# Kernel tuning notes

Measured on AMD Instinct MI355X. Metric: run time of the kernel, lower is better.

Reference implementation:

```python
import jax, jax.numpy as jnp
import numpy as np

BEV_H, BEV_W, BEV_Z = 128, 128, 16
N_VOX = BEV_H * BEV_W * BEV_Z  # 262144
C = 128
N_UNMASKED = N_VOX // 4       # 65536 seed voxels (proposal > 0)
LN_EPS = 1e-5
NEG_SLOPE = 0.01


def setup_inputs() -> dict:
    key = jax.random.key(0)
    ks = jax.random.split(key, 8)
    x3d = jax.random.normal(ks[0], (1, C, N_VOX), dtype=jnp.float32)
    # disjoint unmasked/masked index sets from a permutation (proposal mask)
    perm = jax.random.permutation(ks[1], N_VOX)
    unmasked_idx = jnp.sort(perm[:N_UNMASKED]).astype(jnp.int32)
    masked_idx = jnp.sort(perm[N_UNMASKED:]).astype(jnp.int32)
    s = 0.05
    return {
        "x3d": x3d,
        "w1": jax.random.normal(ks[2], (C, C // 2), jnp.float32) * s,
        "b1": jnp.zeros((C // 2,), jnp.float32),
        "ln_g": jnp.ones((C // 2,), jnp.float32),
        "ln_b": jnp.zeros((C // 2,), jnp.float32),
        "w2": jax.random.normal(ks[3], (C // 2, C), jnp.float32) * s,
        "b2": jnp.zeros((C,), jnp.float32),
        "sdb_w": jax.random.normal(ks[4], (C, C // 2), jnp.float32) * s,
        "sdb_b": jnp.zeros((C // 2,), jnp.float32),
        "ssc_w": jax.random.normal(ks[5], (C // 2, 20), jnp.float32) * s,
        "ssc_b": jnp.zeros((20,), jnp.float32),
        "aux_w": jax.random.normal(ks[6], (C, 20), jnp.float32) * s,
        "aux_b": jnp.zeros((20,), jnp.float32),
        "unmasked_idx": unmasked_idx,
        "masked_idx": masked_idx,
    }


def _leaky(x):
    return jnp.where(x > 0, x, NEG_SLOPE * x)


def _layernorm(x, g, b):
    mu = jnp.mean(x, axis=-1, keepdims=True)
    var = jnp.mean(jnp.square(x - mu), axis=-1, keepdims=True)
    return (x - mu) * jax.lax.rsqrt(var + LN_EPS) * g + b


def reference(x3d, w1, b1, ln_g, ln_b, w2, b2, sdb_w, sdb_b, ssc_w, ssc_b,
              aux_w, aux_b, unmasked_idx, masked_idx):
    feats = x3d[0].T  # [N_vox, C]
    # gather seed (unmasked) voxel features; SGB treated as identity stand-in
    seed_feats = feats[unmasked_idx]            # [Nu, C]
    # gather masked voxel features and infill with mlp_prior:
    # Linear -> LayerNorm -> LeakyReLU -> Linear
    m = feats[masked_idx]                       # [Nm, C]
    h = _leaky(_layernorm(m @ w1 + b1, ln_g, ln_b))
    prior = h @ w2 + b2                         # [Nm, C]
    # scatter both into the dense voxel grid
    vox = jnp.zeros((N_VOX, C), x3d.dtype)
    vox = vox.at[unmasked_idx].set(seed_feats).at[masked_idx].set(prior)
    # SDB dense decode stand-in: pointwise conv C -> C/2 + LeakyReLU
    d = _leaky(vox @ sdb_w + sdb_b)             # [N_vox, C/2]
    # ssc head: per-voxel logits -> [1, 20, H, W, Z]
    ssc = d @ ssc_w + ssc_b                     # [N_vox, 20]
    ssc_logit = ssc.reshape(BEV_H, BEV_W, BEV_Z, 20).transpose(3, 0, 1, 2)[None]
    # aux sparse head on seed features
    sem_logit = seed_feats @ aux_w + aux_b      # [Nu, 20]
    return ssc_logit, sem_logit
```

## Files before the change

kernel.cpp:

```cpp
#include <hip/hip_runtime.h>
#include <hip/hip_bf16.h>


#define NVOX 262144
#define NU   65536
#define NM   196608
#define CIN  128
#define CHALF 64
#define NCLS 20
#define TR   64
#define NBLK (NVOX / TR)

#define SXS 136
#define SHS 68
#define SOS 21

#define W1F  0
#define W2F  8192
#define SDBF 16384
#define SSCF 24576
#define AUXF 26624
#define WS_WT 30720

typedef unsigned short u16;
typedef short    bf16x4 __attribute__((ext_vector_type(4)));
typedef short    bf16x8 __attribute__((ext_vector_type(8)));
typedef float    f32x4  __attribute__((ext_vector_type(4)));

__device__ __forceinline__ u16 f2b(float f) {
    __hip_bfloat16 h = __float2bfloat16(f);
    return *(u16*)&h;
}

__global__ void prep_weights(const float* __restrict__ w1,  const float* __restrict__ w2,
                             const float* __restrict__ sdbw,const float* __restrict__ sscw,
                             const float* __restrict__ auxw,
                             const int* __restrict__ uidx,  const int* __restrict__ midx,
                             u16* __restrict__ ws) {
    int i = blockIdx.x * blockDim.x + threadIdx.x;
    const int stride = gridDim.x * blockDim.x;
    int* __restrict__ rank = (int*)(ws + WS_WT);
    for (int t = i; t < NU; t += stride) rank[uidx[t]] = t;
    for (int t = i; t < NM; t += stride) rank[midx[t]] = -1;
    for (; i < WS_WT; i += stride) {
        float v;
        if (i < W2F) {
            int t = i, j = t & 7, lane = (t >> 3) & 63, kc = (t >> 9) & 3, nt = t >> 11;
            int k = kc*32 + (lane >> 4)*8 + j, n = nt*16 + (lane & 15);
            v = w1[k*CHALF + n];
        } else if (i < SDBF) {
            int t = i - W2F, j = t & 7, lane = (t >> 3) & 63, kc = (t >> 9) & 1, nt = t >> 10;
            int k = kc*32 + (lane >> 4)*8 + j, n = nt*16 + (lane & 15);
            v = w2[k*CIN + n];
        } else if (i < SSCF) {
            int t = i - SDBF, j = t & 7, lane = (t >> 3) & 63, kc = (t >> 9) & 3, nt = t >> 11;
            int k = kc*32 + (lane >> 4)*8 + j, n = nt*16 + (lane & 15);
            v = sdbw[k*CHALF + n];
        } else if (i < AUXF) {
            int t = i - SSCF, j = t & 7, lane = (t >> 3) & 63, kc = (t >> 9) & 1, nt = t >> 10;
            int k = kc*32 + (lane >> 4)*8 + j, n = nt*16 + (lane & 15);
            v = (n < NCLS) ? sscw[k*NCLS + n] : 0.f;
        } else {
            int t = i - AUXF, j = t & 7, lane = (t >> 3) & 63, kc = (t >> 9) & 3, nt = t >> 11;
            int k = kc*32 + (lane >> 4)*8 + j, n = nt*16 + (lane & 15);
            v = (n < NCLS) ? auxw[k*NCLS + n] : 0.f;
        }
        ws[i] = f2b(v);
    }
}

__global__ __launch_bounds__(512, 8)
void sgn_mfma(const float* __restrict__ x3d,
              const float* __restrict__ b1,   const float* __restrict__ lng,
              const float* __restrict__ lnb,  const float* __restrict__ bb2,
              const float* __restrict__ sdbb, const float* __restrict__ sscb,
              const float* __restrict__ auxb,
              const int* __restrict__ rank,   const u16* __restrict__ wt,
              float* __restrict__ out)
{
    __shared__ __align__(16) u16 sX[TR * SXS];
    __shared__ __align__(16) u16 sH[TR * SHS];
    __shared__ __align__(16) float sOut[TR * SOS];
    __shared__ float sLN[TR][2][2];
    __shared__ int sRank[TR];

    const int tid = threadIdx.x;
    const int p0  = (int)blockIdx.x * TR;

    {
        const int gch = (tid >> 4) * 4;
        const int vp  = (tid & 15) * 4;
        f32x4 cv[4];
        #pragma unroll
        for (int r = 0; r < 4; ++r)
            cv[r] = *(const f32x4*)&x3d[(size_t)(gch + r) * NVOX + p0 + vp];
        #pragma unroll
        for (int j = 0; j < 4; ++j) {
            bf16x4 row;
            #pragma unroll
            for (int r = 0; r < 4; ++r) ((u16*)&row)[r] = f2b(cv[r][j]);
            *(bf16x4*)&sX[(vp + j) * SXS + gch] = row;
        }
    }
    if (tid < TR) sRank[tid] = rank[p0 + tid];
    __syncthreads();

    const int w    = tid >> 6;
    const int half = w & 1;
    const int m0   = (w >> 1) * 16;
    const int lane = tid & 63;
    const int q    = lane >> 4;
    const int n15  = lane & 15;
    const int kq   = q * 8;

    {
        const int ntb = half * 2;
        f32x4 acc[2];
        #pragma unroll
        for (int i = 0; i < 2; ++i) {
            const float b = b1[(ntb + i)*16 + n15];
            acc[i] = (f32x4){b, b, b, b};
        }
        bf16x8 af[4];
        #pragma unroll
        for (int kc = 0; kc < 4; ++kc)
            af[kc] = *(const bf16x8*)&sX[(m0 + n15) * SXS + kc*32 + kq];
        #pragma unroll
        for (int h2 = 0; h2 < 2; ++h2) {
            bf16x8 bf[4];
            #pragma unroll
            for (int kk = 0; kk < 2; ++kk)
                #pragma unroll
                for (int i = 0; i < 2; ++i)
                    bf[kk*2 + i] = *(const bf16x8*)&wt[W1F + (((ntb+i)*4 + (2*h2+kk))*64 + lane)*8];
            #pragma unroll
            for (int kk = 0; kk < 2; ++kk)
                #pragma unroll
                for (int i = 0; i < 2; ++i)
                    acc[i] = __builtin_amdgcn_mfma_f32_16x16x32_bf16(af[2*h2+kk], bf[kk*2+i], acc[i], 0, 0, 0);
        }
        float s1v[4], s2v[4];
        #pragma unroll
        for (int reg = 0; reg < 4; ++reg) {
            float s1 = acc[0][reg] + acc[1][reg];
            float s2 = acc[0][reg]*acc[0][reg] + acc[1][reg]*acc[1][reg];
            #pragma unroll
            for (int m = 1; m <= 8; m <<= 1) {
                s1 += __shfl_xor(s1, m, 64);
                s2 += __shfl_xor(s2, m, 64);
            }
            s1v[reg] = s1; s2v[reg] = s2;
        }
        if (n15 == 0) {
            #pragma unroll
            for (int reg = 0; reg < 4; ++reg) {
                const int row = m0 + q*4 + reg;
                sLN[row][half][0] = s1v[reg];
                sLN[row][half][1] = s2v[reg];
            }
        }
        __syncthreads();
        float gv[2], ev[2];
        #pragma unroll
        for (int i = 0; i < 2; ++i) { gv[i] = lng[(ntb+i)*16 + n15]; ev[i] = lnb[(ntb+i)*16 + n15]; }
        #pragma unroll
        for (int reg = 0; reg < 4; ++reg) {
            const int row = m0 + q*4 + reg;
            const float s1 = s1v[reg] + sLN[row][half^1][0];
            const float s2 = s2v[reg] + sLN[row][half^1][1];
            const float mu  = s1 * (1.f/64.f);
            const float var = s2 * (1.f/64.f) - mu*mu;
            const float rs  = rsqrtf(var + 1e-5f);
            #pragma unroll
            for (int i = 0; i < 2; ++i) {
                float h = (acc[i][reg] - mu) * rs * gv[i] + ev[i];
                h = h > 0.f ? h : 0.01f*h;
                sH[row * SHS + (ntb+i)*16 + n15] = f2b(h);
            }
        }
    }
    __syncthreads();

    {
        const int ntb2 = half * 4;
        f32x4 acc2[4];
        #pragma unroll
        for (int i = 0; i < 4; ++i) {
            const float b = bb2[(ntb2 + i)*16 + n15];
            acc2[i] = (f32x4){b, b, b, b};
        }
        bf16x8 af2[2];
        #pragma unroll
        for (int kc = 0; kc < 2; ++kc)
            af2[kc] = *(const bf16x8*)&sH[(m0 + n15) * SHS + kc*32 + kq];
        #pragma unroll
        for (int kc = 0; kc < 2; ++kc) {
            bf16x8 bf[4];
            #pragma unroll
            for (int i = 0; i < 4; ++i)
                bf[i] = *(const bf16x8*)&wt[W2F + (((ntb2+i)*2 + kc)*64 + lane)*8];
            #pragma unroll
            for (int i = 0; i < 4; ++i)
                acc2[i] = __builtin_amdgcn_mfma_f32_16x16x32_bf16(af2[kc], bf[i], acc2[i], 0, 0, 0);
        }
        #pragma unroll
        for (int reg = 0; reg < 4; ++reg) {
            const int row = m0 + q*4 + reg;
            if (sRank[row] < 0) {
                #pragma unroll
                for (int i = 0; i < 4; ++i)
                    sX[row * SXS + (ntb2+i)*16 + n15] = f2b(acc2[i][reg]);
            }
        }
    }
    __syncthreads();

    {
        const int ntb = half * 2;
        f32x4 accd[2];
        #pragma unroll
        for (int i = 0; i < 2; ++i) {
            const float b = sdbb[(ntb + i)*16 + n15];
            accd[i] = (f32x4){b, b, b, b};
        }
        bf16x8 af[4];
        #pragma unroll
        for (int kc = 0; kc < 4; ++kc)
            af[kc] = *(const bf16x8*)&sX[(m0 + n15) * SXS + kc*32 + kq];
        #pragma unroll
        for (int h2 = 0; h2 < 2; ++h2) {
            bf16x8 bf[4];
            #pragma unroll
            for (int kk = 0; kk < 2; ++kk)
                #pragma unroll
                for (int i = 0; i < 2; ++i)
                    bf[kk*2 + i] = *(const bf16x8*)&wt[SDBF + (((ntb+i)*4 + (2*h2+kk))*64 + lane)*8];
            #pragma unroll
            for (int kk = 0; kk < 2; ++kk)
                #pragma unroll
                for (int i = 0; i < 2; ++i)
                    accd[i] = __builtin_amdgcn_mfma_f32_16x16x32_bf16(af[2*h2+kk], bf[kk*2+i], accd[i], 0, 0, 0);
        }
        #pragma unroll
        for (int reg = 0; reg < 4; ++reg) {
            const int row = m0 + q*4 + reg;
            #pragma unroll
            for (int i = 0; i < 2; ++i) {
                float vv = accd[i][reg];
                vv = vv > 0.f ? vv : 0.01f*vv;
                sH[row * SHS + (ntb+i)*16 + n15] = f2b(vv);
            }
        }
    }
    __syncthreads();

    {
        f32x4 accs;
        {
            const int col = half*16 + n15;
            const float b = (col < NCLS) ? sscb[col] : 0.f;
            accs = (f32x4){b, b, b, b};
        }
        bf16x8 af2[2];
        #pragma unroll
        for (int kc = 0; kc < 2; ++kc)
            af2[kc] = *(const bf16x8*)&sH[(m0 + n15) * SHS + kc*32 + kq];
        bf16x8 bf[2];
        #pragma unroll
        for (int kc = 0; kc < 2; ++kc)
            bf[kc] = *(const bf16x8*)&wt[SSCF + ((half*2 + kc)*64 + lane)*8];
        #pragma unroll
        for (int kc = 0; kc < 2; ++kc)
            accs = __builtin_amdgcn_mfma_f32_16x16x32_bf16(af2[kc], bf[kc], accs, 0, 0, 0);
        #pragma unroll
        for (int reg = 0; reg < 4; ++reg) {
            const int row = m0 + q*4 + reg;
            if (half == 0)      sOut[row*SOS + n15] = accs[reg];
            else if (n15 < 4)   sOut[row*SOS + 16 + n15] = accs[reg];
        }
    }

    {
        f32x4 acca;
        {
            const int col = half*16 + n15;
            const float b = (col < NCLS) ? auxb[col] : 0.f;
            acca = (f32x4){b, b, b, b};
        }
        bf16x8 af[4];
        #pragma unroll
        for (int kc = 0; kc < 4; ++kc)
            af[kc] = *(const bf16x8*)&sX[(m0 + n15) * SXS + kc*32 + kq];
        bf16x8 bf[4];
        #pragma unroll
        for (int kc = 0; kc < 4; ++kc)
            bf[kc] = *(const bf16x8*)&wt[AUXF + ((half*4 + kc)*64 + lane)*8];
        #pragma unroll
        for (int kc = 0; kc < 4; ++kc)
            acca = __builtin_amdgcn_mfma_f32_16x16x32_bf16(af[kc], bf[kc], acca, 0, 0, 0);
        const size_t abase = (size_t)NCLS * NVOX;
        #pragma unroll
        for (int reg = 0; reg < 4; ++reg) {
            const int rk = sRank[m0 + q*4 + reg];
            if (rk >= 0) {
                if (half == 0)      out[abase + (size_t)rk * NCLS + n15] = acca[reg];
                else if (n15 < 4)   out[abase + (size_t)rk * NCLS + 16 + n15] = acca[reg];
            }
        }
    }
    __syncthreads();

    #pragma unroll
    for (int jj = 0; jj < 2; ++jj) {
        const int i = tid + jj*512;
        out[(size_t)(i >> 6) * NVOX + p0 + (i & 63)] = sOut[(i & 63) * SOS + (i >> 6)];
    }
    {
        const int i = tid + 1024;
        if (i < 1280)
            out[(size_t)(i >> 6) * NVOX + p0 + (i & 63)] = sOut[(i & 63) * SOS + (i >> 6)];
    }
}

extern "C" void kernel_launch(void* const* d_in, const int* in_sizes, int n_in,
                              void* d_out, int out_size, void* d_ws, size_t ws_size,
                              hipStream_t stream) {
    const float* x3d  = (const float*)d_in[0];
    const float* w1   = (const float*)d_in[1];
    const float* b1   = (const float*)d_in[2];
    const float* lng  = (const float*)d_in[3];
    const float* lnb  = (const float*)d_in[4];
    const float* w2   = (const float*)d_in[5];
    const float* bb2  = (const float*)d_in[6];
    const float* sdbw = (const float*)d_in[7];
    const float* sdbb = (const float*)d_in[8];
    const float* sscw = (const float*)d_in[9];
    const float* sscb = (const float*)d_in[10];
    const float* auxw = (const float*)d_in[11];
    const float* auxb = (const float*)d_in[12];
    const int*   uidx = (const int*)d_in[13];
    const int*   midx = (const int*)d_in[14];
    float* out = (float*)d_out;
    u16*   wt  = (u16*)d_ws;
    const int* rank = (const int*)((const char*)d_ws + WS_WT*2);

    hipLaunchKernelGGL(prep_weights, dim3(128), dim3(256), 0, stream,
                       w1, w2, sdbw, sscw, auxw, uidx, midx, wt);
    hipLaunchKernelGGL(sgn_mfma, dim3(NBLK), dim3(512), 0, stream,
                       x3d, b1, lng, lnb, bb2, sdbb, sscb, auxb,
                       rank, wt, out);
}
```

Measured before the change: 249.5 us.

## Make blocks persistent over 16 tiles with weights held in registers

Each block now loops over 16 consecutive 64-voxel tiles instead of handling one. All bf16 weight fragments and biases are loaded into registers once per block and reused across the tiles, so per-tile global weight loads go away. The launch bounds occupancy hint drops from 8 to 2 so the larger register footprint fits. The trade-offs are fewer blocks (256), lower occupancy, and serialized load/compute per tile with no prefetch, which could leave memory latency exposed.

```diff
diff --git a/kernel.cpp b/kernel.cpp
--- a/kernel.cpp
+++ b/kernel.cpp
@@ -9,7 +9,8 @@
 #define CHALF 64
 #define NCLS 20
 #define TR   64
-#define NBLK (NVOX / TR)
+#define TILES 16
+#define NBLK (NVOX / (TR * TILES))
 
 #define SXS 136
 #define SHS 68
@@ -69,7 +70,7 @@
     }
 }
 
-__global__ __launch_bounds__(512, 8)
+__global__ __launch_bounds__(512, 2)
 void sgn_mfma(const float* __restrict__ x3d,
               const float* __restrict__ b1,   const float* __restrict__ lng,
               const float* __restrict__ lnb,  const float* __restrict__ bb2,
@@ -84,26 +85,8 @@
     __shared__ float sLN[TR][2][2];
     __shared__ int sRank[TR];
 
-    const int tid = threadIdx.x;
-    const int p0  = (int)blockIdx.x * TR;
-
-    {
-        const int gch = (tid >> 4) * 4;
-        const int vp  = (tid & 15) * 4;
-        f32x4 cv[4];
-        #pragma unroll
-        for (int r = 0; r < 4; ++r)
-            cv[r] = *(const f32x4*)&x3d[(size_t)(gch + r) * NVOX + p0 + vp];
-        #pragma unroll
-        for (int j = 0; j < 4; ++j) {
-            bf16x4 row;
-            #pragma unroll
-            for (int r = 0; r < 4; ++r) ((u16*)&row)[r] = f2b(cv[r][j]);
-            *(bf16x4*)&sX[(vp + j) * SXS + gch] = row;
-        }
-    }
-    if (tid < TR) sRank[tid] = rank[p0 + tid];
-    __syncthreads();
+    const int tid  = threadIdx.x;
+    const int base = (int)blockIdx.x * (TR * TILES);
 
     const int w    = tid >> 6;
     const int half = w & 1;
@@ -113,212 +96,216 @@
     const int n15  = lane & 15;
     const int kq   = q * 8;
 
-    {
-        const int ntb = half * 2;
-        f32x4 acc[2];
+    const int ntb  = half * 2;
+    const int ntb2 = half * 4;
+    bf16x8 w1r[8], w2r[8], sdbr[8], sscr[2], auxr[4];
+    #pragma unroll
+    for (int i = 0; i < 2; ++i)
         #pragma unroll
-        for (int i = 0; i < 2; ++i) {
-            const float b = b1[(ntb + i)*16 + n15];
-            acc[i] = (f32x4){b, b, b, b};
-        }
-        bf16x8 af[4];
-        #pragma unroll
-        for (int kc = 0; kc < 4; ++kc)
-            af[kc] = *(const bf16x8*)&sX[(m0 + n15) * SXS + kc*32 + kq];
-        #pragma unroll
-        for (int h2 = 0; h2 < 2; ++h2) {
-            bf16x8 bf[4];
-            #pragma unroll
-            for (int kk = 0; kk < 2; ++kk)
-                #pragma unroll
-                for (int i = 0; i < 2; ++i)
-                    bf[kk*2 + i] = *(const bf16x8*)&wt[W1F + (((ntb+i)*4 + (2*h2+kk))*64 + lane)*8];
-            #pragma unroll
-            for (int kk = 0; kk < 2; ++kk)
-                #pragma unroll
-                for (int i = 0; i < 2; ++i)
-                    acc[i] = __builtin_amdgcn_mfma_f32_16x16x32_bf16(af[2*h2+kk], bf[kk*2+i], acc[i], 0, 0, 0);
-        }
-        float s1v[4], s2v[4];
-        #pragma unroll
-        for (int reg = 0; reg < 4; ++reg) {
-            float s1 = acc[0][reg] + acc[1][reg];
-            float s2 = acc[0][reg]*acc[0][reg] + acc[1][reg]*acc[1][reg];
-            #pragma unroll
-            for (int m = 1; m <= 8; m <<= 1) {
-                s1 += __shfl_xor(s1, m, 64);
-                s2 += __shfl_xor(s2, m, 64);
-            }
-            s1v[reg] = s1; s2v[reg] = s2;
-        }
-        if (n15 == 0) {
-            #pragma unroll
-            for (int reg = 0; reg < 4; ++reg) {
-                const int row = m0 + q*4 + reg;
-                sLN[row][half][0] = s1v[reg];
-                sLN[row][half][1] = s2v[reg];
-            }
-        }
-        __syncthreads();
-        float gv[2], ev[2];
-        #pragma unroll
-        for (int i = 0; i < 2; ++i) { gv[i] = lng[(ntb+i)*16 + n15]; ev[i] = lnb[(ntb+i)*16 + n15]; }
-        #pragma unroll
-        for (int reg = 0; reg < 4; ++reg) {
-            const int row = m0 + q*4 + reg;
-            const float s1 = s1v[reg] + sLN[row][half^1][0];
-            const float s2 = s2v[reg] + sLN[row][half^1][1];
-            const float mu  = s1 * (1.f/64.f);
-            const float var = s2 * (1.f/64.f) - mu*mu;
-            const float rs  = rsqrtf(var + 1e-5f);
-            #pragma unroll
-            for (int i = 0; i < 2; ++i) {
-                float h = (acc[i][reg] - mu) * rs * gv[i] + ev[i];
-                h = h > 0.f ? h : 0.01f*h;
-                sH[row * SHS + (ntb+i)*16 + n15] = f2b(h);
-            }
-        }
-    }
-    __syncthreads();
-
-    {
-        const int ntb2 = half * 4;
-        f32x4 acc2[4];
-        #pragma unroll
-        for (int i = 0; i < 4; ++i) {
-            const float b = bb2[(ntb2 + i)*16 + n15];
-            acc2[i] = (f32x4){b, b, b, b};
-        }
-        bf16x8 af2[2];
+        for (int kc = 0; kc < 4; ++kc) {
+            w1r [i*4 + kc] = *(const bf16x8*)&wt[W1F  + (((ntb+i)*4 + kc)*64 + lane)*8];
+            sdbr[i*4 + kc] = *(const bf16x8*)&wt[SDBF + (((ntb+i)*4 + kc)*64 + lane)*8];
+        }
+    #pragma unroll
+    for (int i = 0; i < 4; ++i)
         #pragma unroll
         for (int kc = 0; kc < 2; ++kc)
-            af2[kc] = *(const bf16x8*)&sH[(m0 + n15) * SHS + kc*32 + kq];
+            w2r[i*2 + kc] = *(const bf16x8*)&wt[W2F + (((ntb2+i)*2 + kc)*64 + lane)*8];
+    #pragma unroll
+    for (int kc = 0; kc < 2; ++kc)
+        sscr[kc] = *(const bf16x8*)&wt[SSCF + ((half*2 + kc)*64 + lane)*8];
+    #pragma unroll
+    for (int kc = 0; kc < 4; ++kc)
+        auxr[kc] = *(const bf16x8*)&wt[AUXF + ((half*4 + kc)*64 + lane)*8];
+
+    float b1v[2], gv[2], ev[2], sdbbv[2], b2v[4];
+    #pragma unroll
+    for (int i = 0; i < 2; ++i) {
+        b1v[i]   = b1  [(ntb+i)*16 + n15];
+        gv[i]    = lng [(ntb+i)*16 + n15];
+        ev[i]    = lnb [(ntb+i)*16 + n15];
+        sdbbv[i] = sdbb[(ntb+i)*16 + n15];
+    }
+    #pragma unroll
+    for (int i = 0; i < 4; ++i) b2v[i] = bb2[(ntb2+i)*16 + n15];
+    const int  colh  = half*16 + n15;
+    const float sscbv = (colh < NCLS) ? sscb[colh] : 0.f;
+    const float auxbv = (colh < NCLS) ? auxb[colh] : 0.f;
+
+    const int gch = (tid >> 4) * 4;
+    const int vp  = (tid & 15) * 4;
+
+    #pragma unroll 1
+    for (int t = 0; t < TILES; ++t) {
+        const int p0 = base + t * TR;
+
+        {
+            f32x4 cv[4];
+            #pragma unroll
+            for (int r = 0; r < 4; ++r)
+                cv[r] = *(const f32x4*)&x3d[(size_t)(gch + r) * NVOX + p0 + vp];
+            #pragma unroll
+            for (int j = 0; j < 4; ++j) {
+                bf16x4 row;
+                #pragma unroll
+                for (int r = 0; r < 4; ++r) ((u16*)&row)[r] = f2b(cv[r][j]);
+                *(bf16x4*)&sX[(vp + j) * SXS + gch] = row;
+            }
+        }
+        if (tid < TR) sRank[tid] = rank[p0 + tid];
+        __syncthreads();
+
+        {
+            f32x4 acc[2];
+            #pragma unroll
+            for (int i = 0; i < 2; ++i) acc[i] = (f32x4){b1v[i], b1v[i], b1v[i], b1v[i]};
+            bf16x8 af[4];
+            #pragma unroll
+            for (int kc = 0; kc < 4; ++kc)
+                af[kc] = *(const bf16x8*)&sX[(m0 + n15) * SXS + kc*32 + kq];
+            #pragma unroll
+            for (int kc = 0; kc < 4; ++kc)
+                #pragma unroll
+                for (int i = 0; i < 2; ++i)
+                    acc[i] = __builtin_amdgcn_mfma_f32_16x16x32_bf16(af[kc], w1r[i*4+kc], acc[i], 0, 0, 0);
+            float s1v[4], s2v[4];
+            #pragma unroll
+            for (int reg = 0; reg < 4; ++reg) {
+                float s1 = acc[0][reg] + acc[1][reg];
+                float s2 = acc[0][reg]*acc[0][reg] + acc[1][reg]*acc[1][reg];
+                #pragma unroll
+                for (int m = 1; m <= 8; m <<= 1) {
+                    s1 += __shfl_xor(s1, m, 64);
+                    s2 += __shfl_xor(s2, m, 64);
+                }
+                s1v[reg] = s1; s2v[reg] = s2;
+            }
+            if (n15 == 0) {
+                #pragma unroll
+                for (int reg = 0; reg < 4; ++reg) {
+                    const int row = m0 + q*4 + reg;
+                    sLN[row][half][0] = s1v[reg];
+                    sLN[row][half][1] = s2v[reg];
+                }
+            }
+            __syncthreads();
+            #pragma unroll
+            for (int reg = 0; reg < 4; ++reg) {
+                const int row = m0 + q*4 + reg;
+                const float s1 = s1v[reg] + sLN[row][half^1][0];
+                const float s2 = s2v[reg] + sLN[row][half^1][1];
+                const float mu  = s1 * (1.f/64.f);
+                const float var = s2 * (1.f/64.f) - mu*mu;
+                const float rs  = rsqrtf(var + 1e-5f);
+                #pragma unroll
+                for (int i = 0; i < 2; ++i) {
+                    float h = (acc[i][reg] - mu) * rs * gv[i] + ev[i];
+                    h = h > 0.f ? h : 0.01f*h;
+                    sH[row * SHS + (ntb+i)*16 + n15] = f2b(h);
+                }
+            }
+        }
+        __syncthreads();
+
+        {
+            f32x4 acc2[4];
+            #pragma unroll
+            for (int i = 0; i < 4; ++i) acc2[i] = (f32x4){b2v[i], b2v[i], b2v[i], b2v[i]};
+            bf16x8 af2[2];
+            #pragma unroll
+            for (int kc = 0; kc < 2; ++kc)
+                af2[kc] = *(const bf16x8*)&sH[(m0 + n15) * SHS + kc*32 + kq];
+            #pragma unroll
+            for (int kc = 0; kc < 2; ++kc)
+                #pragma unroll
+                for (int i = 0; i < 4; ++i)
+                    acc2[i] = __builtin_amdgcn_mfma_f32_16x16x32_bf16(af2[kc], w2r[i*2+kc], acc2[i], 0, 0, 0);
+            #pragma unroll
+            for (int reg = 0; reg < 4; ++reg) {
+                const int row = m0 + q*4 + reg;
+                if (sRank[row] < 0) {
+                    #pragma unroll
+                    for (int i = 0; i < 4; ++i)
+                        sX[row * SXS + (ntb2+i)*16 + n15] = f2b(acc2[i][reg]);
+                }
+            }
+        }
+        __syncthreads();
+
+        {
+            f32x4 accd[2];
+            #pragma unroll
+            for (int i = 0; i < 2; ++i) accd[i] = (f32x4){sdbbv[i], sdbbv[i], sdbbv[i], sdbbv[i]};
+            bf16x8 af[4];
+            #pragma unroll
+            for (int kc = 0; kc < 4; ++kc)
+                af[kc] = *(const bf16x8*)&sX[(m0 + n15) * SXS + kc*32 + kq];
+            #pragma unroll
+            for (int kc = 0; kc < 4; ++kc)
+                #pragma unroll
+                for (int i = 0; i < 2; ++i)
+                    accd[i] = __builtin_amdgcn_mfma_f32_16x16x32_bf16(af[kc], sdbr[i*4+kc], accd[i], 0, 0, 0);
+            #pragma unroll
+            for (int reg = 0; reg < 4; ++reg) {
+                const int row = m0 + q*4 + reg;
+                #pragma unroll
+                for (int i = 0; i < 2; ++i) {
+                    float vv = accd[i][reg];
+                    vv = vv > 0.f ? vv : 0.01f*vv;
+                    sH[row * SHS + (ntb+i)*16 + n15] = f2b(vv);
+                }
+            }
+        }
+        __syncthreads();
+
+        {
+            f32x4 accs = (f32x4){sscbv, sscbv, sscbv, sscbv};
+            bf16x8 af2[2];
+            #pragma unroll
+            for (int kc = 0; kc < 2; ++kc)
+                af2[kc] = *(const bf16x8*)&sH[(m0 + n15) * SHS + kc*32 + kq];
+            #pragma unroll
+            for (int kc = 0; kc < 2; ++kc)
+                accs = __builtin_amdgcn_mfma_f32_16x16x32_bf16(af2[kc], sscr[kc], accs, 0, 0, 0);
+            #pragma unroll
+            for (int reg = 0; reg < 4; ++reg) {
+                const int row = m0 + q*4 + reg;
+                if (half == 0)      sOut[row*SOS + n15] = accs[reg];
+                else if (n15 < 4)   sOut[row*SOS + 16 + n15] = accs[reg];
+            }
+        }
+
+        {
+            f32x4 acca = (f32x4){auxbv, auxbv, auxbv, auxbv};
+            bf16x8 af[4];
+            #pragma unroll
+            for (int kc = 0; kc < 4; ++kc)
+                af[kc] = *(const bf16x8*)&sX[(m0 + n15) * SXS + kc*32 + kq];
+            #pragma unroll
+            for (int kc = 0; kc < 4; ++kc)
+                acca = __builtin_amdgcn_mfma_f32_16x16x32_bf16(af[kc], auxr[kc], acca, 0, 0, 0);
+            const size_t abase = (size_t)NCLS * NVOX;
+            #pragma unroll
+            for (int reg = 0; reg < 4; ++reg) {
+                const int rk = sRank[m0 + q*4 + reg];
+                if (rk >= 0) {
+                    if (half == 0)      out[abase + (size_t)rk * NCLS + n15] = acca[reg];
+                    else if (n15 < 4)   out[abase + (size_t)rk * NCLS + 16 + n15] = acca[reg];
+                }
+            }
+        }
+        __syncthreads();
+
         #pragma unroll
-        for (int kc = 0; kc < 2; ++kc) {
-            bf16x8 bf[4];
-            #pragma unroll
-            for (int i = 0; i < 4; ++i)
-                bf[i] = *(const bf16x8*)&wt[W2F + (((ntb2+i)*2 + kc)*64 + lane)*8];
-            #pragma unroll
-            for (int i = 0; i < 4; ++i)
-                acc2[i] = __builtin_amdgcn_mfma_f32_16x16x32_bf16(af2[kc], bf[i], acc2[i], 0, 0, 0);
-        }
-        #pragma unroll
-        for (int reg = 0; reg < 4; ++reg) {
-            const int row = m0 + q*4 + reg;
-            if (sRank[row] < 0) {
-                #pragma unroll
-                for (int i = 0; i < 4; ++i)
-                    sX[row * SXS + (ntb2+i)*16 + n15] = f2b(acc2[i][reg]);
-            }
-        }
-    }
-    __syncthreads();
-
-    {
-        const int ntb = half * 2;
-        f32x4 accd[2];
-        #pragma unroll
-        for (int i = 0; i < 2; ++i) {
-            const float b = sdbb[(ntb + i)*16 + n15];
-            accd[i] = (f32x4){b, b, b, b};
-        }
-        bf16x8 af[4];
-        #pragma unroll
-        for (int kc = 0; kc < 4; ++kc)
-            af[kc] = *(const bf16x8*)&sX[(m0 + n15) * SXS + kc*32 + kq];
-        #pragma unroll
-        for (int h2 = 0; h2 < 2; ++h2) {
-            bf16x8 bf[4];
-            #pragma unroll
-            for (int kk = 0; kk < 2; ++kk)
-                #pragma unroll
-                for (int i = 0; i < 2; ++i)
-                    bf[kk*2 + i] = *(const bf16x8*)&wt[SDBF + (((ntb+i)*4 + (2*h2+kk))*64 + lane)*8];
-            #pragma unroll
-            for (int kk = 0; kk < 2; ++kk)
-                #pragma unroll
-                for (int i = 0; i < 2; ++i)
-                    accd[i] = __builtin_amdgcn_mfma_f32_16x16x32_bf16(af[2*h2+kk], bf[kk*2+i], accd[i], 0, 0, 0);
-        }
-        #pragma unroll
-        for (int reg = 0; reg < 4; ++reg) {
-            const int row = m0 + q*4 + reg;
-            #pragma unroll
-            for (int i = 0; i < 2; ++i) {
-                float vv = accd[i][reg];
-                vv = vv > 0.f ? vv : 0.01f*vv;
-                sH[row * SHS + (ntb+i)*16 + n15] = f2b(vv);
-            }
-        }
-    }
-    __syncthreads();
-
-    {
-        f32x4 accs;
-        {
-            const int col = half*16 + n15;
-            const float b = (col < NCLS) ? sscb[col] : 0.f;
-            accs = (f32x4){b, b, b, b};
-        }
-        bf16x8 af2[2];
-        #pragma unroll
-        for (int kc = 0; kc < 2; ++kc)
-            af2[kc] = *(const bf16x8*)&sH[(m0 + n15) * SHS + kc*32 + kq];
-        bf16x8 bf[2];
-        #pragma unroll
-        for (int kc = 0; kc < 2; ++kc)
-            bf[kc] = *(const bf16x8*)&wt[SSCF + ((half*2 + kc)*64 + lane)*8];
-        #pragma unroll
-        for (int kc = 0; kc < 2; ++kc)
-            accs = __builtin_amdgcn_mfma_f32_16x16x32_bf16(af2[kc], bf[kc], accs, 0, 0, 0);
-        #pragma unroll
-        for (int reg = 0; reg < 4; ++reg) {
-            const int row = m0 + q*4 + reg;
-            if (half == 0)      sOut[row*SOS + n15] = accs[reg];
-            else if (n15 < 4)   sOut[row*SOS + 16 + n15] = accs[reg];
-        }
-    }
-
-    {
-        f32x4 acca;
-        {
-            const int col = half*16 + n15;
-            const float b = (col < NCLS) ? auxb[col] : 0.f;
-            acca = (f32x4){b, b, b, b};
-        }
-        bf16x8 af[4];
-        #pragma unroll
-        for (int kc = 0; kc < 4; ++kc)
-            af[kc] = *(const bf16x8*)&sX[(m0 + n15) * SXS + kc*32 + kq];
-        bf16x8 bf[4];
-        #pragma unroll
-        for (int kc = 0; kc < 4; ++kc)
-            bf[kc] = *(const bf16x8*)&wt[AUXF + ((half*4 + kc)*64 + lane)*8];
-        #pragma unroll
-        for (int kc = 0; kc < 4; ++kc)
-            acca = __builtin_amdgcn_mfma_f32_16x16x32_bf16(af[kc], bf[kc], acca, 0, 0, 0);
-        const size_t abase = (size_t)NCLS * NVOX;
-        #pragma unroll
-        for (int reg = 0; reg < 4; ++reg) {
-            const int rk = sRank[m0 + q*4 + reg];
-            if (rk >= 0) {
-                if (half == 0)      out[abase + (size_t)rk * NCLS + n15] = acca[reg];
-                else if (n15 < 4)   out[abase + (size_t)rk * NCLS + 16 + n15] = acca[reg];
-            }
-        }
-    }
-    __syncthreads();
-
-    #pragma unroll
-    for (int jj = 0; jj < 2; ++jj) {
-        const int i = tid + jj*512;
-        out[(size_t)(i >> 6) * NVOX + p0 + (i & 63)] = sOut[(i & 63) * SOS + (i >> 6)];
-    }
-    {
-        const int i = tid + 1024;
-        if (i < 1280)
+        for (int jj = 0; jj < 2; ++jj) {
+            const int i = tid + jj*512;
             out[(size_t)(i >> 6) * NVOX + p0 + (i & 63)] = sOut[(i & 63) * SOS + (i >> 6)];
+        }
+        {
+            const int i = tid + 1024;
+            if (i < 1280)
+                out[(size_t)(i >> 6) * NVOX + p0 + (i & 63)] = sOut[(i & 63) * SOS + (i >> 6)];
+        }
     }
 }
 
```

Result: slower. 265.2 us (+6.3%).
